# Kernel tuning notes

Measured on AMD Instinct MI355X. Metric: run time of the kernel, lower is better.

Reference implementation:

```python
import jax, jax.numpy as jnp
import numpy as np

B, T, C = 4, 2048, 1024
H, D = 16, 64          # n_head, head_dim; H*D == C
FFN = 4096
EPS = 1e-6


def rmsnorm(x, w):
    rms = jnp.sqrt(jnp.mean(x * x, axis=-1, keepdims=True) + EPS)
    return x / rms * w


def l2norm(x):
    n = jnp.sqrt(jnp.sum(x * x, axis=-1, keepdims=True))
    return x / jnp.maximum(n, 1e-12)


def setup_inputs() -> dict:
    key = jax.random.key(0)
    ks = jax.random.split(key, 16)
    s = 0.02
    inp = {
        'x': jax.random.normal(ks[0], (B, T, C), jnp.float32),
        'cos': jax.random.uniform(ks[1], (T, D // 2), jnp.float32),
        'sin': jax.random.uniform(ks[2], (T, D // 2), jnp.float32),
        'norm1_w': jnp.ones((C,), jnp.float32),
        'norm2_w': jnp.ones((C,), jnp.float32),
        'q_w': jax.random.normal(ks[3], (C, C), jnp.float32) * s,
        'k_w': jax.random.normal(ks[4], (C, C), jnp.float32) * s,
        'v_w': jax.random.normal(ks[5], (C, C), jnp.float32) * s,
        'beta_w': jax.random.normal(ks[6], (H, C), jnp.float32) * s,
        'beta_b': jnp.zeros((H,), jnp.float32),
        'gate_w': jax.random.normal(ks[7], (C, C), jnp.float32) * s,
        'o_w': jax.random.normal(ks[8], (C, C), jnp.float32) * s,
        'ffn_gate_w': jax.random.normal(ks[9], (FFN, C), jnp.float32) * s,
        'ffn_up_w': jax.random.normal(ks[10], (FFN, C), jnp.float32) * s,
        'ffn_down_w': jax.random.normal(ks[11], (C, FFN), jnp.float32) * s,
    }
    return inp


def gated_delta_net(xn, q_w, k_w, v_w, beta_w, beta_b, gate_w, o_w):
    # projections -> (B, T, H, D)
    q = (xn @ q_w.T).reshape(B, T, H, D)
    k = (xn @ k_w.T).reshape(B, T, H, D)
    v = (xn @ v_w.T).reshape(B, T, H, D)
    beta = jax.nn.sigmoid(xn @ beta_w.T + beta_b)   # (B, T, H)
    gate = jax.nn.sigmoid(xn @ gate_w.T)            # (B, T, C)
    q = l2norm(q)
    k = l2norm(k)

    # time-major for scan: (T, B, H, D)
    qs = jnp.moveaxis(q, 1, 0)
    ks = jnp.moveaxis(k, 1, 0)
    vs = jnp.moveaxis(v, 1, 0)
    bs = jnp.moveaxis(beta, 1, 0)                   # (T, B, H)

    def step(M, inp):
        q_t, k_t, v_t, b_t = inp
        o_t = jnp.einsum('bhdc,bhc->bhd', M, q_t)
        dv = v_t - jnp.einsum('bhdc,bhc->bhd', M, k_t)
        M = M + b_t[:, :, None, None] * jnp.einsum('bhd,bhc->bhdc', dv, k_t)
        return M, o_t

    M0 = jnp.zeros((B, H, D, D), xn.dtype)
    _, os = jax.lax.scan(step, M0, (qs, ks, vs, bs))  # os: (T, B, H, D)
    o = jnp.moveaxis(os, 0, 1).reshape(B, T, C)
    return (gate * o) @ o_w.T


def swiglu(xn, gate_w, up_w, down_w):
    return (jax.nn.silu(xn @ gate_w.T) * (xn @ up_w.T)) @ down_w.T


def reference(x, cos, sin, norm1_w, norm2_w, q_w, k_w, v_w, beta_w, beta_b,
              gate_w, o_w, ffn_gate_w, ffn_up_w, ffn_down_w):
    # layer_idx=0 -> GatedDeltaNet branch (cos/sin unused, as in torch module)
    x = x + gated_delta_net(rmsnorm(x, norm1_w), q_w, k_w, v_w,
                            beta_w, beta_b, gate_w, o_w)
    x = x + swiglu(rmsnorm(x, norm2_w), ffn_gate_w, ffn_up_w, ffn_down_w)
    return x
```

## Files before the change

kernel.cpp:

```cpp
#include <hip/hip_runtime.h>
#include <stdint.h>

typedef unsigned short u16;
typedef unsigned int   u32;
typedef unsigned long long u64;

typedef __bf16 bf16x8 __attribute__((ext_vector_type(8)));
typedef u16    u16x8  __attribute__((ext_vector_type(8)));
typedef u16    u16x4  __attribute__((ext_vector_type(4)));
typedef float  f32x4  __attribute__((ext_vector_type(4)));

#define BQ 4
#define TT 2048
#define CC 1024
#define HH 16
#define DD 64
#define FF 4096
#define BT 8192
#define NCH 32
#define LCH 64
#define LS 72
#define SE 140

__device__ __forceinline__ float b2f(u16 v) {
  u32 u = ((u32)v) << 16;
  return __builtin_bit_cast(float, u);
}
__device__ __forceinline__ u16 f2b(float f) {
  u32 u = __builtin_bit_cast(u32, f);
  u32 r = (u + 0x7fffu + ((u >> 16) & 1u)) >> 16;
  return (u16)r;
}
__device__ __forceinline__ bf16x8 ld8(const u16* p) {
  return __builtin_bit_cast(bf16x8, *(const u16x8*)p);
}
__device__ __forceinline__ float sigmoidf_(float x) {
  return 1.0f / (1.0f + __expf(-x));
}

#define MFMA16(a, b, c) __builtin_amdgcn_mfma_f32_16x16x32_bf16(a, b, c, 0, 0, 0)

__device__ __forceinline__ void stage16(const u16* g, u16* lds_base) {
  __builtin_amdgcn_global_load_lds(
      (const __attribute__((address_space(1))) u32*)(uintptr_t)g,
      (__attribute__((address_space(3))) u32*)lds_base, 16, 0, 0);
}

struct Cvt { const float* src; u16* dst; u32 n; u32 pad; };
struct CvtArgs { Cvt d[12]; };

__global__ __launch_bounds__(256) void convert_k(CvtArgs a)
{
  const Cvt c = a.d[blockIdx.y];
  u64 i = ((u64)blockIdx.x * 256 + threadIdx.x) * 8;
  if (i >= c.n) return;
  f32x4 v0 = *(const f32x4*)(c.src + i);
  f32x4 v1 = *(const f32x4*)(c.src + i + 4);
  u16x8 o;
#pragma unroll
  for (int e = 0; e < 4; ++e) { o[e] = f2b(v0[e]); o[e + 4] = f2b(v1[e]); }
  *(u16x8*)(c.dst + i) = o;
}

template <int MODE>
__global__ __launch_bounds__(256) void gemm_bt(
    const u16* __restrict__ A, const u16* __restrict__ Bw,
    void* __restrict__ Cv, const void* __restrict__ res,
    int M, int N, int K)
{
  __shared__ __align__(16) u16 smem[128 * SE];
  const int tid  = threadIdx.x;
  const int lane = tid & 63;
  const int wave = tid >> 6;
  const int bm = blockIdx.x, bn = blockIdx.y;
  const int rw = lane >> 2;
  const int kq = (lane & 3) * 8;
  const int lo = lane & 15;
  const int quad = lane >> 4;
  const int wm = wave & 1, wn = wave >> 1;

  const u16* Ag = A  + (u64)(bm * 128 + wave * 16 + rw) * K + kq;
  const u16* Bg = Bw + (u64)(bn * 128 + wave * 16 + rw) * K + kq;
  u16* const Ab[2] = { smem + wave * 512, smem + 4096 + wave * 512 };
  u16* const Bb[2] = { smem + 8192 + wave * 512, smem + 12288 + wave * 512 };

  f32x4 acc[4][4] = {};
  const int niter = K >> 5;

  stage16(Ag, Ab[0]);
  stage16(Ag + (u64)64 * K, Ab[0] + 2048);
  stage16(Bg, Bb[0]);
  stage16(Bg + (u64)64 * K, Bb[0] + 2048);

  int cur = 0;
  for (int it = 0; it < niter; ++it) {
    __syncthreads();
    if (it + 1 < niter) {
      int kn = (it + 1) << 5;
      stage16(Ag + kn, Ab[cur ^ 1]);
      stage16(Ag + (u64)64 * K + kn, Ab[cur ^ 1] + 2048);
      stage16(Bg + kn, Bb[cur ^ 1]);
      stage16(Bg + (u64)64 * K + kn, Bb[cur ^ 1] + 2048);
    }
    const u16* Ac = smem + cur * 4096;
    const u16* Bc = smem + 8192 + cur * 4096;
    bf16x8 af[4], bq[4];
#pragma unroll
    for (int i = 0; i < 4; ++i)
      af[i] = ld8(Ac + (wm * 64 + i * 16 + lo) * 32 + quad * 8);
#pragma unroll
    for (int j = 0; j < 4; ++j)
      bq[j] = ld8(Bc + (wn * 64 + j * 16 + lo) * 32 + quad * 8);
#pragma unroll
    for (int i = 0; i < 4; ++i)
#pragma unroll
      for (int j = 0; j < 4; ++j)
        acc[i][j] = MFMA16(af[i], bq[j], acc[i][j]);
    cur ^= 1;
  }

  if (MODE == 2) {
    const u16* R16 = (const u16*)res;
    float* C32 = (float*)Cv;
#pragma unroll
    for (int i = 0; i < 4; ++i)
#pragma unroll
      for (int j = 0; j < 4; ++j)
#pragma unroll
        for (int r = 0; r < 4; ++r) {
          int row = bm * 128 + wm * 64 + i * 16 + quad * 4 + r;
          int col = bn * 128 + wn * 64 + j * 16 + lo;
          u64 off = (u64)row * N + col;
          C32[off] = acc[i][j][r] + b2f(R16[off]);
        }
    return;
  }

  __syncthreads();
#pragma unroll
  for (int i = 0; i < 4; ++i)
#pragma unroll
    for (int j = 0; j < 4; ++j)
#pragma unroll
      for (int r = 0; r < 4; ++r)
        smem[(wm * 64 + i * 16 + quad * 4 + r) * SE + wn * 64 + j * 16 + lo] =
            f2b(acc[i][j][r]);
  __syncthreads();

  u16* C16 = (u16*)Cv;
  const float* R32 = (const float*)res;
  const u16* R16 = (const u16*)res;
  const int orow = tid >> 4, ocol = (tid & 15) * 8;
#pragma unroll
  for (int w = 0; w < 8; ++w) {
    int rl = orow + w * 16;
    u16x8 v = *(const u16x8*)(smem + rl * SE + ocol);
    u64 off = (u64)(bm * 128 + rl) * N + bn * 128 + ocol;
    if (MODE == 0) {
      *(u16x8*)(C16 + off) = v;
    } else if (MODE == 1) {
      f32x4 r0 = *(const f32x4*)(R32 + off);
      f32x4 r1 = *(const f32x4*)(R32 + off + 4);
      u16x8 o;
#pragma unroll
      for (int e = 0; e < 4; ++e) {
        o[e]     = f2b(b2f(v[e])     + r0[e]);
        o[e + 4] = f2b(b2f(v[e + 4]) + r1[e]);
      }
      *(u16x8*)(C16 + off) = o;
    } else {
      u16x8 g = *(const u16x8*)(R16 + off);
      u16x8 o;
#pragma unroll
      for (int e = 0; e < 8; ++e) {
        float gg = b2f(g[e]);
        o[e] = f2b(gg * sigmoidf_(gg) * b2f(v[e]));
      }
      *(u16x8*)(C16 + off) = o;
    }
  }
}

template <int IN32>
__global__ __launch_bounds__(256) void rmsnorm_k(
    const void* __restrict__ xv, const u16* __restrict__ w, u16* __restrict__ out)
{
  __shared__ float red[4];
  const int row = blockIdx.x, tid = threadIdx.x;
  float v0, v1, v2, v3;
  if (IN32) {
    f32x4 raw = *(const f32x4*)((const float*)xv + (u64)row * CC + tid * 4);
    v0 = raw[0]; v1 = raw[1]; v2 = raw[2]; v3 = raw[3];
  } else {
    u16x4 raw = *(const u16x4*)((const u16*)xv + (u64)row * CC + tid * 4);
    v0 = b2f(raw[0]); v1 = b2f(raw[1]); v2 = b2f(raw[2]); v3 = b2f(raw[3]);
  }
  float s = v0 * v0 + v1 * v1 + v2 * v2 + v3 * v3;
#pragma unroll
  for (int m = 1; m < 64; m <<= 1) s += __shfl_xor(s, m, 64);
  if ((tid & 63) == 0) red[tid >> 6] = s;
  __syncthreads();
  float tot = red[0] + red[1] + red[2] + red[3];
  float r = rsqrtf(tot * (1.0f / CC) + 1e-6f);
  const u16* wr = w + tid * 4;
  u16x4 o;
  o[0] = f2b(v0 * r * b2f(wr[0]));
  o[1] = f2b(v1 * r * b2f(wr[1]));
  o[2] = f2b(v2 * r * b2f(wr[2]));
  o[3] = f2b(v3 * r * b2f(wr[3]));
  *(u16x4*)(out + (u64)row * CC + tid * 4) = o;
}

__global__ __launch_bounds__(256) void l2norm_k(u16* __restrict__ q)
{
  const int row = blockIdx.x, tid = threadIdx.x;
  const int hh = tid >> 4, ss = tid & 15;
  u16* p = q + (u64)row * CC + hh * DD + ss * 4;
  u16x4 raw = *(const u16x4*)p;
  float v0 = b2f(raw[0]), v1 = b2f(raw[1]), v2 = b2f(raw[2]), v3 = b2f(raw[3]);
  float s = v0 * v0 + v1 * v1 + v2 * v2 + v3 * v3;
#pragma unroll
  for (int m = 1; m < 16; m <<= 1) s += __shfl_xor(s, m, 64);
  float sc = 1.0f / fmaxf(sqrtf(s), 1e-12f);
  u16x4 o;
  o[0] = f2b(v0 * sc); o[1] = f2b(v1 * sc);
  o[2] = f2b(v2 * sc); o[3] = f2b(v3 * sc);
  *(u16x4*)p = o;
}

__global__ __launch_bounds__(256) void beta_k(
    const u16* __restrict__ xn, const u16* __restrict__ bw,
    const u16* __restrict__ bb, float* __restrict__ beta)
{
  const int row = blockIdx.x, tid = threadIdx.x;
  const int hh = tid >> 4, ss = tid & 15;
  const u16* xr = xn + (u64)row * CC + ss * 64;
  const u16* wr = bw + (u64)hh * CC + ss * 64;
  float s = 0.f;
#pragma unroll
  for (int j = 0; j < 8; ++j) {
    u16x8 a = *(const u16x8*)(xr + j * 8);
    u16x8 c = *(const u16x8*)(wr + j * 8);
#pragma unroll
    for (int e = 0; e < 8; ++e) s += b2f(a[e]) * b2f(c[e]);
  }
#pragma unroll
  for (int m = 1; m < 16; m <<= 1) s += __shfl_xor(s, m, 64);
  if (ss == 0) beta[(u64)row * HH + hh] = sigmoidf_(s + b2f(bb[hh]));
}

__global__ __launch_bounds__(256) void chunk_pre(
    const u16* __restrict__ qn, const u16* __restrict__ kn,
    const u16* __restrict__ vn, const float* __restrict__ beta,
    u16* __restrict__ wneg, u16* __restrict__ u0m, u16* __restrict__ pm)
{
  __shared__ __align__(16) u16 Qc[64 * LS], Kc[64 * LS], Vc[64 * LS];
  __shared__ float Af[64 * 64];
  __shared__ float bet[64];
  const int tid = threadIdx.x;
  const int lane = tid & 63, wave = tid >> 6;
  const int lo = lane & 15, quad = lane >> 4;
  const int bc = blockIdx.x;
  const int bh = bc >> 5, c = bc & 31;
  const int b = bh >> 4, h = bh & 15;
  const u64 gbase = ((u64)(b * TT + c * LCH) * HH + h) * DD;
  const u64 cb = (u64)bc * 4096;

#pragma unroll
  for (int it = 0; it < 2; ++it) {
    int idx = tid + it * 256;
    int t = idx >> 3, seg = (idx & 7) * 8;
    u64 g = gbase + (u64)t * CC + seg;
    *(u16x8*)(Qc + t * LS + seg) = *(const u16x8*)(qn + g);
    *(u16x8*)(Kc + t * LS + seg) = *(const u16x8*)(kn + g);
    *(u16x8*)(Vc + t * LS + seg) = *(const u16x8*)(vn + g);
  }
  if (tid < 64) bet[tid] = beta[(u64)(b * TT + c * LCH + tid) * HH + h];
  __syncthreads();

  {
    const int wm = wave & 1, wn = wave >> 1;
    f32x4 aa[2][2] = {};
#pragma unroll
    for (int k0 = 0; k0 < 64; k0 += 32) {
      bf16x8 af[2], bq[2];
#pragma unroll
      for (int i = 0; i < 2; ++i) af[i] = ld8(Kc + (wm * 32 + i * 16 + lo) * LS + k0 + quad * 8);
#pragma unroll
      for (int j = 0; j < 2; ++j) bq[j] = ld8(Kc + (wn * 32 + j * 16 + lo) * LS + k0 + quad * 8);
#pragma unroll
      for (int i = 0; i < 2; ++i)
#pragma unroll
        for (int j = 0; j < 2; ++j) aa[i][j] = MFMA16(af[i], bq[j], aa[i][j]);
    }
#pragma unroll
    for (int i = 0; i < 2; ++i)
#pragma unroll
      for (int j = 0; j < 2; ++j)
#pragma unroll
        for (int r = 0; r < 4; ++r) {
          int t = wm * 32 + i * 16 + quad * 4 + r;
          int s = wn * 32 + j * 16 + lo;
          Af[t * 64 + s] = (s < t) ? bet[t] * aa[i][j][r] : 0.0f;
        }
  }
  __syncthreads();

  if (wave < 2) {
    const u16* src = (wave == 0) ? Kc : Vc;
    u16* dst = (wave == 0) ? wneg : u0m;
    const float sgn = (wave == 0) ? -1.0f : 1.0f;
    const int d = lane;
    float hist[64];
#pragma unroll
    for (int t = 0; t < 64; ++t) {
      float a = bet[t] * b2f(src[t * LS + d]);
#pragma unroll
      for (int s = 0; s < t; ++s) a -= Af[t * 64 + s] * hist[s];
      hist[t] = a;
      dst[cb + (u64)t * 64 + d] = f2b(sgn * a);
    }
  } else {
    const int w2 = wave - 2;
    f32x4 ap[2][4] = {};
#pragma unroll
    for (int k0 = 0; k0 < 64; k0 += 32) {
      bf16x8 af[2], bq[4];
#pragma unroll
      for (int i = 0; i < 2; ++i) af[i] = ld8(Qc + (w2 * 32 + i * 16 + lo) * LS + k0 + quad * 8);
#pragma unroll
      for (int j = 0; j < 4; ++j) bq[j] = ld8(Kc + (j * 16 + lo) * LS + k0 + quad * 8);
#pragma unroll
      for (int i = 0; i < 2; ++i)
#pragma unroll
        for (int j = 0; j < 4; ++j) ap[i][j] = MFMA16(af[i], bq[j], ap[i][j]);
    }
#pragma unroll
    for (int i = 0; i < 2; ++i)
#pragma unroll
      for (int j = 0; j < 4; ++j)
#pragma unroll
        for (int r = 0; r < 4; ++r) {
          int t = w2 * 32 + i * 16 + quad * 4 + r;
          int s = j * 16 + lo;
          pm[cb + (u64)t * 64 + s] = f2b((s < t) ? ap[i][j][r] : 0.0f);
        }
  }
}

__global__ __launch_bounds__(256) void chunk_seq(
    const u16* __restrict__ qn, const u16* __restrict__ kn,
    const u16* __restrict__ wneg, const u16* __restrict__ u0m,
    const u16* __restrict__ pm, const u16* __restrict__ gate,
    u16* __restrict__ ob)
{
  __shared__ __align__(16) u16 Qs[64 * LS], KTs[64 * LS], Ws[64 * LS], Ps[64 * LS];
  __shared__ __align__(16) u16 U0q[64 * 16];
  __shared__ __align__(16) u16 Sq[16 * LS], UTq[16 * LS];
  const int tid = threadIdx.x;
  const int lane = tid & 63, wave = tid >> 6;
  const int lo = lane & 15, quad = lane >> 4;
  const int blk = blockIdx.x;
  const int bh = blk >> 2, q = blk & 3;
  const int b = bh >> 4, h = bh & 15;
  f32x4 Sacc = {};

  for (int i = tid; i < 16 * LS; i += 256) Sq[i] = 0;
  __syncthreads();

#pragma unroll 1
  for (int c = 0; c < NCH; ++c) {
    const u64 gbase = ((u64)(b * TT + c * LCH) * HH + h) * DD;
    const u64 cb = (u64)(bh * NCH + c) * 4096;
#pragma unroll
    for (int it = 0; it < 2; ++it) {
      int idx = tid + it * 256;
      int t = idx >> 3, seg = (idx & 7) * 8;
      u64 g = gbase + (u64)t * CC + seg;
      *(u16x8*)(Qs + t * LS + seg) = *(const u16x8*)(qn + g);
      u16x8 kv = *(const u16x8*)(kn + g);
#pragma unroll
      for (int jj = 0; jj < 8; ++jj) KTs[(seg + jj) * LS + t] = kv[jj];
      *(u16x8*)(Ws + t * LS + seg) = *(const u16x8*)(wneg + cb + t * 64 + seg);
      *(u16x8*)(Ps + t * LS + seg) = *(const u16x8*)(pm + cb + t * 64 + seg);
    }
    if (tid < 128) {
      int t = tid >> 1, half = (tid & 1) * 8;
      *(u16x8*)(U0q + t * 16 + half) =
          *(const u16x8*)(u0m + cb + t * 64 + q * 16 + half);
    }
    __syncthreads();

    f32x4 au;
#pragma unroll
    for (int r = 0; r < 4; ++r)
      au[r] = b2f(U0q[(wave * 16 + quad * 4 + r) * 16 + lo]);
#pragma unroll
    for (int k0 = 0; k0 < 64; k0 += 32) {
      bf16x8 af = ld8(Ws + (wave * 16 + lo) * LS + k0 + quad * 8);
      bf16x8 bq = ld8(Sq + lo * LS + k0 + quad * 8);
      au = MFMA16(af, bq, au);
    }
#pragma unroll
    for (int r = 0; r < 4; ++r)
      UTq[lo * LS + wave * 16 + quad * 4 + r] = f2b(au[r]);
    __syncthreads();

    f32x4 ao = {};
#pragma unroll
    for (int k0 = 0; k0 < 64; k0 += 32) {
      bf16x8 af = ld8(Qs + (wave * 16 + lo) * LS + k0 + quad * 8);
      bf16x8 bq = ld8(Sq + lo * LS + k0 + quad * 8);
      ao = MFMA16(af, bq, ao);
    }
#pragma unroll
    for (int k0 = 0; k0 < 64; k0 += 32) {
      bf16x8 af = ld8(Ps + (wave * 16 + lo) * LS + k0 + quad * 8);
      bf16x8 bq = ld8(UTq + lo * LS + k0 + quad * 8);
      ao = MFMA16(af, bq, ao);
    }
#pragma unroll
    for (int r = 0; r < 4; ++r) {
      u64 gidx = gbase + (u64)(wave * 16 + quad * 4 + r) * CC + q * 16 + lo;
      float gg = b2f(gate[gidx]);
      ob[gidx] = f2b(sigmoidf_(gg) * ao[r]);
    }

#pragma unroll
    for (int k0 = 0; k0 < 64; k0 += 32) {
      bf16x8 af = ld8(UTq + lo * LS + k0 + quad * 8);
      bf16x8 bq = ld8(KTs + (wave * 16 + lo) * LS + k0 + quad * 8);
      Sacc = MFMA16(af, bq, Sacc);
    }
    __syncthreads();
#pragma unroll
    for (int r = 0; r < 4; ++r)
      Sq[(quad * 4 + r) * LS + wave * 16 + lo] = f2b(Sacc[r]);
    __syncthreads();
  }
}

extern "C" void kernel_launch(void* const* d_in, const int* in_sizes, int n_in,
                              void* d_out, int out_size, void* d_ws, size_t ws_size,
                              hipStream_t stream)
{
  (void)in_sizes; (void)n_in; (void)out_size; (void)ws_size;
  const float* x32 = (const float*)d_in[0];
  char* ws = (char*)d_ws;
  const u64 SZ = (u64)BT * CC * 2;
  const u64 MB = 1ull << 20;

  u16* xn1  = (u16*)(ws + 0 * SZ);
  u16* qb   = (u16*)(ws + 1 * SZ);
  u16* kb   = (u16*)(ws + 2 * SZ);
  u16* vb   = (u16*)(ws + 3 * SZ);
  u16* grw  = (u16*)(ws + 4 * SZ);
  u16* wneg = (u16*)(ws + 5 * SZ);
  u16* u0m  = (u16*)(ws + 6 * SZ);
  u16* pmm  = (u16*)(ws + 7 * SZ);
  u16* obf  = (u16*)(ws + 8 * SZ);
  u16* x2   = (u16*)(ws + 9 * SZ);
  float* beta = (float*)(ws + 10 * SZ);
  char* CV  = ws + 10 * SZ + MB;
  u16* qwc  = (u16*)(CV + 0 * MB);
  u16* kwc  = (u16*)(CV + 2 * MB);
  u16* vwc  = (u16*)(CV + 4 * MB);
  u16* gwc  = (u16*)(CV + 6 * MB);
  u16* owc  = (u16*)(CV + 8 * MB);
  u16* fgwc = (u16*)(CV + 10 * MB);
  u16* fuwc = (u16*)(CV + 18 * MB);
  u16* fdwc = (u16*)(CV + 26 * MB);
  u16* bwc  = (u16*)(CV + 34 * MB);
  u16* n1c  = (u16*)(CV + 34 * MB + 64 * 1024);
  u16* n2c  = (u16*)(CV + 34 * MB + 80 * 1024);
  u16* bbc  = (u16*)(CV + 34 * MB + 96 * 1024);
  u16* ffg  = (u16*)(ws + 0 * SZ);
  u16* xn2  = obf;

  dim3 blk(256);
  dim3 g1(BT / 128, CC / 128);
  dim3 g2(BT / 128, FF / 128);

  CvtArgs ca;
  ca.d[0]  = { (const float*)d_in[5],  qwc,  (u32)(CC * CC), 0 };
  ca.d[1]  = { (const float*)d_in[6],  kwc,  (u32)(CC * CC), 0 };
  ca.d[2]  = { (const float*)d_in[7],  vwc,  (u32)(CC * CC), 0 };
  ca.d[3]  = { (const float*)d_in[10], gwc,  (u32)(CC * CC), 0 };
  ca.d[4]  = { (const float*)d_in[11], owc,  (u32)(CC * CC), 0 };
  ca.d[5]  = { (const float*)d_in[12], fgwc, (u32)(FF * CC), 0 };
  ca.d[6]  = { (const float*)d_in[13], fuwc, (u32)(FF * CC), 0 };
  ca.d[7]  = { (const float*)d_in[14], fdwc, (u32)(CC * FF), 0 };
  ca.d[8]  = { (const float*)d_in[8],  bwc,  (u32)(HH * CC), 0 };
  ca.d[9]  = { (const float*)d_in[3],  n1c,  (u32)CC, 0 };
  ca.d[10] = { (const float*)d_in[4],  n2c,  (u32)CC, 0 };
  ca.d[11] = { (const float*)d_in[9],  bbc,  (u32)HH, 0 };
  convert_k<<<dim3(2048, 12), blk, 0, stream>>>(ca);

  rmsnorm_k<1><<<BT, blk, 0, stream>>>(x32, n1c, xn1);
  gemm_bt<0><<<g1, blk, 0, stream>>>(xn1, qwc, qb, nullptr, BT, CC, CC);
  gemm_bt<0><<<g1, blk, 0, stream>>>(xn1, kwc, kb, nullptr, BT, CC, CC);
  gemm_bt<0><<<g1, blk, 0, stream>>>(xn1, vwc, vb, nullptr, BT, CC, CC);
  gemm_bt<0><<<g1, blk, 0, stream>>>(xn1, gwc, grw, nullptr, BT, CC, CC);
  beta_k<<<BT, blk, 0, stream>>>(xn1, bwc, bbc, beta);
  l2norm_k<<<BT, blk, 0, stream>>>(qb);
  l2norm_k<<<BT, blk, 0, stream>>>(kb);
  chunk_pre<<<BQ * HH * NCH, blk, 0, stream>>>(qb, kb, vb, beta, wneg, u0m, pmm);
  chunk_seq<<<BQ * HH * 4, blk, 0, stream>>>(qb, kb, wneg, u0m, pmm, grw, obf);
  gemm_bt<1><<<g1, blk, 0, stream>>>(obf, owc, x2, x32, BT, CC, CC);
  rmsnorm_k<0><<<BT, blk, 0, stream>>>(x2, n2c, xn2);
  gemm_bt<0><<<g2, blk, 0, stream>>>(xn2, fgwc, ffg, nullptr, BT, FF, CC);
  gemm_bt<3><<<g2, blk, 0, stream>>>(xn2, fuwc, ffg, ffg, BT, FF, CC);
  gemm_bt<2><<<g1, blk, 0, stream>>>(ffg, fdwc, d_out, x2, BT, CC, FF);
}
```

Baseline: 767.0 us.

## Add 256x128-tile GEMM, fuse Q/K/V/gate projections, coalesce fp32 residual epilogue

Adds a gemm_bt2 kernel with 256x128 output tiles (8x4 MFMA accumulators per wave, two blocks per CU). It is used for the FFN gate and up projections. The same kernel with a split epilogue replaces the four separate Q/K/V/gate projection launches with one launch. That launch treats the four contiguous weight matrices as a single N=4096 weight and scatters each column block to its projection's output buffer. The down-projection epilogue now stages fp32 results through shared memory in two halves, so residual reads and fp32 stores are vectorised and coalesced. The aim is more operand reuse per tile and fewer launches, at the cost of higher register pressure and a dependence on the weight and output buffers being laid out contiguously.

```diff
diff --git a/kernel.cpp b/kernel.cpp
--- a/kernel.cpp
+++ b/kernel.cpp
@@ -21,6 +21,7 @@
 #define LCH 64
 #define LS 72
 #define SE 140
+#define FS 132
 
 __device__ __forceinline__ float b2f(u16 v) {
   u32 u = ((u32)v) << 16;
@@ -119,24 +120,41 @@
     cur ^= 1;
   }
 
+  __syncthreads();
   if (MODE == 2) {
+    float* Fsm = (float*)smem;
+    float* C32 = (float*)Cv;
     const u16* R16 = (const u16*)res;
-    float* C32 = (float*)Cv;
-#pragma unroll
-    for (int i = 0; i < 4; ++i)
-#pragma unroll
-      for (int j = 0; j < 4; ++j)
-#pragma unroll
-        for (int r = 0; r < 4; ++r) {
-          int row = bm * 128 + wm * 64 + i * 16 + quad * 4 + r;
-          int col = bn * 128 + wn * 64 + j * 16 + lo;
-          u64 off = (u64)row * N + col;
-          C32[off] = acc[i][j][r] + b2f(R16[off]);
-        }
+#pragma unroll
+    for (int hh = 0; hh < 2; ++hh) {
+      if (wm == hh) {
+#pragma unroll
+        for (int i = 0; i < 4; ++i)
+#pragma unroll
+          for (int j = 0; j < 4; ++j)
+#pragma unroll
+            for (int r = 0; r < 4; ++r)
+              Fsm[(i * 16 + quad * 4 + r) * FS + wn * 64 + j * 16 + lo] =
+                  acc[i][j][r];
+      }
+      __syncthreads();
+      const int r2 = tid >> 5, c2 = (tid & 31) * 4;
+#pragma unroll
+      for (int w = 0; w < 8; ++w) {
+        int rl = r2 + w * 8;
+        f32x4 v = *(const f32x4*)(Fsm + rl * FS + c2);
+        u64 off = (u64)(bm * 128 + hh * 64 + rl) * N + bn * 128 + c2;
+        u16x4 rr = *(const u16x4*)(R16 + off);
+        f32x4 o;
+#pragma unroll
+        for (int e = 0; e < 4; ++e) o[e] = v[e] + b2f(rr[e]);
+        *(f32x4*)(C32 + off) = o;
+      }
+      __syncthreads();
+    }
     return;
   }
 
-  __syncthreads();
 #pragma unroll
   for (int i = 0; i < 4; ++i)
 #pragma unroll
@@ -149,35 +167,124 @@
 
   u16* C16 = (u16*)Cv;
   const float* R32 = (const float*)res;
-  const u16* R16 = (const u16*)res;
   const int orow = tid >> 4, ocol = (tid & 15) * 8;
 #pragma unroll
   for (int w = 0; w < 8; ++w) {
     int rl = orow + w * 16;
     u16x8 v = *(const u16x8*)(smem + rl * SE + ocol);
     u64 off = (u64)(bm * 128 + rl) * N + bn * 128 + ocol;
-    if (MODE == 0) {
-      *(u16x8*)(C16 + off) = v;
-    } else if (MODE == 1) {
-      f32x4 r0 = *(const f32x4*)(R32 + off);
-      f32x4 r1 = *(const f32x4*)(R32 + off + 4);
-      u16x8 o;
-#pragma unroll
-      for (int e = 0; e < 4; ++e) {
-        o[e]     = f2b(b2f(v[e])     + r0[e]);
-        o[e + 4] = f2b(b2f(v[e + 4]) + r1[e]);
+    f32x4 r0 = *(const f32x4*)(R32 + off);
+    f32x4 r1 = *(const f32x4*)(R32 + off + 4);
+    u16x8 o;
+#pragma unroll
+    for (int e = 0; e < 4; ++e) {
+      o[e]     = f2b(b2f(v[e])     + r0[e]);
+      o[e + 4] = f2b(b2f(v[e + 4]) + r1[e]);
+    }
+    *(u16x8*)(C16 + off) = o;
+  }
+}
+
+template <int MODE, int SPLIT>
+__global__ __launch_bounds__(256, 2) void gemm_bt2(
+    const u16* __restrict__ A, const u16* __restrict__ Bw,
+    u16* __restrict__ C, const u16* __restrict__ res,
+    int M, int N, int K)
+{
+  __shared__ __align__(16) u16 smem[24576];
+  const int tid  = threadIdx.x;
+  const int lane = tid & 63;
+  const int wave = tid >> 6;
+  const int bm = blockIdx.x, bn = blockIdx.y;
+  const int rw = lane >> 2;
+  const int kq = (lane & 3) * 8;
+  const int lo = lane & 15;
+  const int quad = lane >> 4;
+  const int wm = wave & 1, wn = wave >> 1;
+
+  const u16* Ag = A  + (u64)(bm * 256 + wave * 16 + rw) * K + kq;
+  const u16* Bg = Bw + (u64)(bn * 128 + wave * 16 + rw) * K + kq;
+  u16* const Ab[2] = { smem + wave * 512, smem + 8192 + wave * 512 };
+  u16* const Bb[2] = { smem + 16384 + wave * 512, smem + 20480 + wave * 512 };
+
+  f32x4 acc[8][4] = {};
+  const int niter = K >> 5;
+
+#pragma unroll
+  for (int r = 0; r < 4; ++r) stage16(Ag + (u64)(64 * r) * K, Ab[0] + r * 2048);
+#pragma unroll
+  for (int r = 0; r < 2; ++r) stage16(Bg + (u64)(64 * r) * K, Bb[0] + r * 2048);
+
+  int cur = 0;
+  for (int it = 0; it < niter; ++it) {
+    __syncthreads();
+    if (it + 1 < niter) {
+      int kn = (it + 1) << 5;
+#pragma unroll
+      for (int r = 0; r < 4; ++r)
+        stage16(Ag + (u64)(64 * r) * K + kn, Ab[cur ^ 1] + r * 2048);
+#pragma unroll
+      for (int r = 0; r < 2; ++r)
+        stage16(Bg + (u64)(64 * r) * K + kn, Bb[cur ^ 1] + r * 2048);
+    }
+    const u16* Ac = smem + cur * 8192;
+    const u16* Bc = smem + 16384 + cur * 4096;
+    bf16x8 af[8], bq[4];
+#pragma unroll
+    for (int i = 0; i < 8; ++i)
+      af[i] = ld8(Ac + (wm * 128 + i * 16 + lo) * 32 + quad * 8);
+#pragma unroll
+    for (int j = 0; j < 4; ++j)
+      bq[j] = ld8(Bc + (wn * 64 + j * 16 + lo) * 32 + quad * 8);
+#pragma unroll
+    for (int i = 0; i < 8; ++i)
+#pragma unroll
+      for (int j = 0; j < 4; ++j)
+        acc[i][j] = MFMA16(af[i], bq[j], acc[i][j]);
+    cur ^= 1;
+  }
+
+  __syncthreads();
+  const int orow = tid >> 4, ocol = (tid & 15) * 8;
+#pragma unroll
+  for (int hh = 0; hh < 2; ++hh) {
+    if (wm == hh) {
+#pragma unroll
+      for (int i = 0; i < 8; ++i)
+#pragma unroll
+        for (int j = 0; j < 4; ++j)
+#pragma unroll
+          for (int r = 0; r < 4; ++r)
+            smem[(i * 16 + quad * 4 + r) * SE + wn * 64 + j * 16 + lo] =
+                f2b(acc[i][j][r]);
+    }
+    __syncthreads();
+#pragma unroll
+    for (int w = 0; w < 8; ++w) {
+      int rl = orow + w * 16;
+      int row = bm * 256 + hh * 128 + rl;
+      u16x8 v = *(const u16x8*)(smem + rl * SE + ocol);
+      if (SPLIT) {
+        int proj = bn >> 3;
+        int colp = (bn & 7) * 128 + ocol;
+        *(u16x8*)(C + (u64)proj * BT * CC + (u64)row * CC + colp) = v;
+      } else {
+        u64 off = (u64)row * N + bn * 128 + ocol;
+        if (MODE == 3) {
+          u16x8 g = *(const u16x8*)(res + off);
+          u16x8 o;
+#pragma unroll
+          for (int e = 0; e < 8; ++e) {
+            float gg = b2f(g[e]);
+            o[e] = f2b(gg * sigmoidf_(gg) * b2f(v[e]));
+          }
+          *(u16x8*)(C + off) = o;
+        } else {
+          *(u16x8*)(C + off) = v;
+        }
       }
-      *(u16x8*)(C16 + off) = o;
-    } else {
-      u16x8 g = *(const u16x8*)(R16 + off);
-      u16x8 o;
-#pragma unroll
-      for (int e = 0; e < 8; ++e) {
-        float gg = b2f(g[e]);
-        o[e] = f2b(gg * sigmoidf_(gg) * b2f(v[e]));
-      }
-      *(u16x8*)(C16 + off) = o;
-    }
+    }
+    __syncthreads();
   }
 }
 
@@ -479,7 +586,7 @@
 
   dim3 blk(256);
   dim3 g1(BT / 128, CC / 128);
-  dim3 g2(BT / 128, FF / 128);
+  dim3 g2(BT / 256, FF / 128);
 
   CvtArgs ca;
   ca.d[0]  = { (const float*)d_in[5],  qwc,  (u32)(CC * CC), 0 };
@@ -497,10 +604,7 @@
   convert_k<<<dim3(2048, 12), blk, 0, stream>>>(ca);
 
   rmsnorm_k<1><<<BT, blk, 0, stream>>>(x32, n1c, xn1);
-  gemm_bt<0><<<g1, blk, 0, stream>>>(xn1, qwc, qb, nullptr, BT, CC, CC);
-  gemm_bt<0><<<g1, blk, 0, stream>>>(xn1, kwc, kb, nullptr, BT, CC, CC);
-  gemm_bt<0><<<g1, blk, 0, stream>>>(xn1, vwc, vb, nullptr, BT, CC, CC);
-  gemm_bt<0><<<g1, blk, 0, stream>>>(xn1, gwc, grw, nullptr, BT, CC, CC);
+  gemm_bt2<0, 1><<<g2, blk, 0, stream>>>(xn1, qwc, qb, nullptr, BT, FF, CC);
   beta_k<<<BT, blk, 0, stream>>>(xn1, bwc, bbc, beta);
   l2norm_k<<<BT, blk, 0, stream>>>(qb);
   l2norm_k<<<BT, blk, 0, stream>>>(kb);
@@ -508,7 +612,7 @@
   chunk_seq<<<BQ * HH * 4, blk, 0, stream>>>(qb, kb, wneg, u0m, pmm, grw, obf);
   gemm_bt<1><<<g1, blk, 0, stream>>>(obf, owc, x2, x32, BT, CC, CC);
   rmsnorm_k<0><<<BT, blk, 0, stream>>>(x2, n2c, xn2);
-  gemm_bt<0><<<g2, blk, 0, stream>>>(xn2, fgwc, ffg, nullptr, BT, FF, CC);
-  gemm_bt<3><<<g2, blk, 0, stream>>>(xn2, fuwc, ffg, ffg, BT, FF, CC);
+  gemm_bt2<0, 0><<<g2, blk, 0, stream>>>(xn2, fgwc, ffg, nullptr, BT, FF, CC);
+  gemm_bt2<3, 0><<<g2, blk, 0, stream>>>(xn2, fuwc, ffg, ffg, BT, FF, CC);
   gemm_bt<2><<<g1, blk, 0, stream>>>(ffg, fdwc, d_out, x2, BT, CC, FF);
 }
```

Result: faster. 734.1 us (-4.3%).
